# Kernel optimization log

Hardware: AMD Instinct MI355X
Metric: run time of the kernel (lower is better)

Reference implementation:

```python
import jax, jax.numpy as jnp
import numpy as np

TAU_M = 20.0
DT = 1.0
V_TH = 1.0
V_RESET = 0.0
ALPHA = float(np.exp(-DT / TAU_M))  # membrane decay per step

B, T, I, H, O = 64, 1024, 128, 512, 10


def spike_fn(v):
    # Heaviside spike; surrogate grad handled in fwdbwd module.
    return (v >= 0.0).astype(v.dtype)


def setup_inputs() -> dict:
    key = jax.random.key(0)
    k = jax.random.split(key, 6)
    x = jax.random.normal(k[0], (B, T, I), dtype=jnp.float32)
    # input_projection: Linear(I, H) -> weight [H, I], bias [H]
    Wi = jax.random.normal(k[1], (H, I), dtype=jnp.float32) * (1.0 / np.sqrt(I))
    bi = jnp.zeros((H,), dtype=jnp.float32)
    # recurrent weight [H, H] (xavier-ish)
    Wr = jax.random.normal(k[2], (H, H), dtype=jnp.float32) * float(np.sqrt(2.0 / (H + H)))
    # readout: Linear(H, O)
    Wo = jax.random.normal(k[3], (O, H), dtype=jnp.float32) * (1.0 / np.sqrt(H))
    bo = jnp.zeros((O,), dtype=jnp.float32)
    return {"x": x, "Wi": Wi, "bi": bi, "Wr": Wr, "Wo": Wo, "bo": bo}


def reference(x, Wi, bi, Wr, Wo, bo):
    # Precompute input projection for all timesteps: [B, T, H]
    x_proj = jnp.einsum('bti,hi->bth', x, Wi) + bi

    def step(carry, cur_t):
        h, spikes_prev = carry
        total_current = cur_t + spikes_prev @ Wr        # [B, H]
        h = ALPHA * h + total_current                    # LIF leak + integrate
        spikes = spike_fn(h - V_TH)                      # threshold
        h = spikes * V_RESET + (1.0 - spikes) * h        # reset on spike
        return (h, spikes), spikes

    h0 = jnp.zeros((x.shape[0], Wr.shape[0]), dtype=x.dtype)
    s0 = jnp.zeros_like(h0)
    (_, _), hidden_states = jax.lax.scan(step, (h0, s0), jnp.swapaxes(x_proj, 0, 1))
    hidden_states = jnp.swapaxes(hidden_states, 0, 1)    # [B, T, H]

    hidden_mean = hidden_states.mean(axis=1)             # rate readout
    output = hidden_mean @ Wo.T + bo                     # [B, O]
    return output, hidden_states
```

## Files before the change

### kernel.cpp

```cpp
#include <hip/hip_runtime.h>


#define ALPHA_F 0.951229424500714f

typedef unsigned int u32x4 __attribute__((ext_vector_type(4)));

__device__ float g_mean[64 * 512];

__global__ __launch_bounds__(256) void xproj_kernel(
    const float* __restrict__ x, const float* __restrict__ Wi,
    const float* __restrict__ bi, float* __restrict__ out)
{
    __shared__ float xs[64][132];
    __shared__ float ws[32][132];

    const int tid = threadIdx.x;
    const int bm = blockIdx.x;
    const int bn = blockIdx.y;

    const float* xb = x  + (size_t)bm * 64 * 128;
    const float* wb = Wi + (size_t)bn * 32 * 128;

    for (int l = 0; l < 8; ++l) {
        int idx = l * 256 + tid;
        int row = idx >> 5, c4 = idx & 31;
        *(float4*)(&xs[row][c4 * 4]) = *(const float4*)(xb + row * 128 + c4 * 4);
    }
    for (int l = 0; l < 4; ++l) {
        int idx = l * 256 + tid;
        int row = idx >> 5, c4 = idx & 31;
        *(float4*)(&ws[row][c4 * 4]) = *(const float4*)(wb + row * 128 + c4 * 4);
    }
    __syncthreads();

    const int txh = tid & 15, txm = tid >> 4;
    const int m0 = txm * 4, h0 = txh * 2;

    float4 acc[4][2];
    #pragma unroll
    for (int mm = 0; mm < 4; ++mm)
        #pragma unroll
        for (int q = 0; q < 2; ++q)
            acc[mm][q] = make_float4(0.f, 0.f, 0.f, 0.f);

    for (int k4 = 0; k4 < 32; ++k4) {
        float4 a[4], b[2];
        #pragma unroll
        for (int mm = 0; mm < 4; ++mm) a[mm] = *(const float4*)(&xs[m0 + mm][k4 * 4]);
        #pragma unroll
        for (int q = 0; q < 2; ++q)    b[q]  = *(const float4*)(&ws[h0 + q][k4 * 4]);
        #pragma unroll
        for (int mm = 0; mm < 4; ++mm) {
            #pragma unroll
            for (int q = 0; q < 2; ++q) {
                float p0 = a[mm].x * b[q].x;
                float p1 = a[mm].y * b[q].y;
                float p2 = a[mm].z * b[q].z;
                float p3 = a[mm].w * b[q].w;
                asm volatile("" : "+v"(p0), "+v"(p1), "+v"(p2), "+v"(p3));
                acc[mm][q].x += p0;
                acc[mm][q].y += p1;
                acc[mm][q].z += p2;
                acc[mm][q].w += p3;
            }
        }
    }

    const int hbase = bn * 32 + h0;
    #pragma unroll
    for (int mm = 0; mm < 4; ++mm) {
        size_t m = (size_t)bm * 64 + m0 + mm;
        float2 o;
        {
            float s01 = acc[mm][0].x + acc[mm][0].y;
            float s23 = acc[mm][0].z + acc[mm][0].w;
            float hs  = s01 + s23;
            o.x = hs + bi[hbase + 0];
        }
        {
            float s01 = acc[mm][1].x + acc[mm][1].y;
            float s23 = acc[mm][1].z + acc[mm][1].w;
            float hs  = s01 + s23;
            o.y = hs + bi[hbase + 1];
        }
        *(float2*)(&out[m * 512 + hbase]) = o;
    }
}

struct C8 { float a, b, c, d, e, f, g, h; };

__device__ __forceinline__ C8 fetch8v(const unsigned int* lst, int cidx,
                                      const char* wbase, int lane4) {
    u32x4 L0 = *(const u32x4*)(lst + cidx * 8);
    u32x4 L1 = *(const u32x4*)(lst + cidx * 8 + 4);
    C8 r;
    r.a = *(const float*)(wbase + (L0.x + lane4));
    r.b = *(const float*)(wbase + (L0.y + lane4));
    r.c = *(const float*)(wbase + (L0.z + lane4));
    r.d = *(const float*)(wbase + (L0.w + lane4));
    r.e = *(const float*)(wbase + (L1.x + lane4));
    r.f = *(const float*)(wbase + (L1.y + lane4));
    r.g = *(const float*)(wbase + (L1.z + lane4));
    r.h = *(const float*)(wbase + (L1.w + lane4));
    return r;
}

__device__ __forceinline__ void consume8(const C8& v, int e, int kA, int k,
                                         float& recA, float& recB) {
    if (e + 8 <= kA) {
        recA += v.a; recA += v.b; recA += v.c; recA += v.d;
        recA += v.e; recA += v.f; recA += v.g; recA += v.h;
    } else if (e >= kA && e + 8 <= k) {
        recB += v.a; recB += v.b; recB += v.c; recB += v.d;
        recB += v.e; recB += v.f; recB += v.g; recB += v.h;
    } else {
        if (e + 0 < k) { if (e + 0 < kA) recA += v.a; else recB += v.a; }
        if (e + 1 < k) { if (e + 1 < kA) recA += v.b; else recB += v.b; }
        if (e + 2 < k) { if (e + 2 < kA) recA += v.c; else recB += v.c; }
        if (e + 3 < k) { if (e + 3 < kA) recA += v.d; else recB += v.d; }
        if (e + 4 < k) { if (e + 4 < kA) recA += v.e; else recB += v.e; }
        if (e + 5 < k) { if (e + 5 < kA) recA += v.f; else recB += v.f; }
        if (e + 6 < k) { if (e + 6 < kA) recA += v.g; else recB += v.g; }
        if (e + 7 < k) { if (e + 7 < kA) recA += v.h; else recB += v.h; }
    }
}

__global__ __launch_bounds__(128, 1) void scan_kernel(
    const float* __restrict__ Wr, float* __restrict__ hid,
    u32x4* __restrict__ syn)
{
    const int blk  = blockIdx.x;
    const int p    = blk & 31;
    const int c    = blk >> 5;
    const int tid  = threadIdx.x;
    const int w    = tid >> 6;
    const int lane = tid & 63;
    const int s    = p + 32 * w;
    const int n    = (c << 6) + lane;
    const int lane4 = lane << 2;

    __shared__ float wrs[512][64];
    __shared__ alignas(16) unsigned int lists[2][512];
    __shared__ alignas(16) unsigned int maskbuf[2][16];

    #pragma unroll
    for (int i = 0; i < 8; ++i) ((unsigned int*)lists)[i * 128 + tid] = 0;

    {
        const float* src = Wr + (c << 6);
        for (int it = 0; it < 64; ++it) {
            int idx = it * 128 + tid;
            int r = idx >> 4, q = idx & 15;
            float4 v = *(const float4*)(src + (size_t)r * 512 + q * 4);
            *(float4*)(&wrs[r][q * 4]) = v;
        }
    }
    __syncthreads();

    unsigned int* list = lists[w];
    const char* wbase = (const char*)&wrs[0][0];
    float* base = hid + ((size_t)s * 1024) * 512 + n;

    float hstate = 0.0f;
    int cnt = 0;
    float xp = base[0];

    u32x4 prb0 = {0, 0, 0, 0}, prb1 = {0, 0, 0, 0};

    for (int t = 0; t < 1024; ++t) {
        int k = 0, kA = 0;
        if (t > 0) {
            const u32x4* pp = syn + ((((t - 1) & 1) * 64 + s) * 8) + (lane >> 3);
            asm volatile("s_waitcnt vmcnt(0)" ::: "memory");
            u32x4 pv;
            asm volatile("global_load_dwordx4 %0, %2, off sc0 sc1\n\t"
                         "global_load_dwordx4 %1, %2, off sc0 sc1"
                         : "+v"(prb0), "+v"(prb1) : "v"(pp) : "memory");
            for (;;) {
                asm volatile("s_waitcnt vmcnt(1)" : "+v"(prb0) :: "memory");
                unsigned long long ok = __ballot(prb0.z == (unsigned)t);
                if (ok == ~0ull) { pv = prb0; break; }
                asm volatile("global_load_dwordx4 %0, %1, off sc0 sc1"
                             : "+v"(prb0) : "v"(pp) : "memory");
                asm volatile("s_waitcnt vmcnt(1)" : "+v"(prb1) :: "memory");
                ok = __ballot(prb1.z == (unsigned)t);
                if (ok == ~0ull) { pv = prb1; break; }
                asm volatile("global_load_dwordx4 %0, %1, off sc0 sc1"
                             : "+v"(prb1) : "v"(pp) : "memory");
            }

            if ((lane & 7) == 0) {
                unsigned long long mword =
                    (((unsigned long long)pv.y) << 32) | (unsigned long long)pv.x;
                *(unsigned long long*)&maskbuf[w][(lane >> 3) * 2] = mword;
            }
            u32x4 r0 = *(const u32x4*)&maskbuf[w][0];
            u32x4 r1 = *(const u32x4*)&maskbuf[w][4];
            u32x4 r2 = *(const u32x4*)&maskbuf[w][8];
            u32x4 r3 = *(const u32x4*)&maskbuf[w][12];

            int p0 = __popc(r0.x), p1 = __popc(r0.y), p2 = __popc(r0.z), p3 = __popc(r0.w);
            int p4 = __popc(r1.x), p5 = __popc(r1.y), p6 = __popc(r1.z), p7 = __popc(r1.w);
            int p8 = __popc(r2.x), p9 = __popc(r2.y), p10 = __popc(r2.z), p11 = __popc(r2.w);
            int p12 = __popc(r3.x), p13 = __popc(r3.y), p14 = __popc(r3.z), p15 = __popc(r3.w);
            int ka_ = p0 + p1 + p2 + p3 + p4 + p5 + p6 + p7 + p8 + p9 + p10 + p11;
            int k_  = ka_ + p12 + p13 + p14 + p15;
            kA = __builtin_amdgcn_readfirstlane(ka_);
            k  = __builtin_amdgcn_readfirstlane(k_);

            const int myW = lane >> 2;
            int pre = 0;
            if (myW >  0) pre += p0;   if (myW >  1) pre += p1;
            if (myW >  2) pre += p2;   if (myW >  3) pre += p3;
            if (myW >  4) pre += p4;   if (myW >  5) pre += p5;
            if (myW >  6) pre += p6;   if (myW >  7) pre += p7;
            if (myW >  8) pre += p8;   if (myW >  9) pre += p9;
            if (myW > 10) pre += p10;  if (myW > 11) pre += p11;
            if (myW > 12) pre += p12;  if (myW > 13) pre += p13;
            if (myW > 14) pre += p14;
            unsigned word = (lane & 4) ? pv.y : pv.x;
            int shb = (lane & 3) * 8;
            pre += __popc(word & ((1u << shb) - 1u));
            unsigned byte = (word >> shb) & 0xFFu;

            int pos = pre;
            unsigned jbase = (unsigned)lane << 11;
            while (byte) {
                int bt = __builtin_ctz(byte);
                byte &= byte - 1u;
                list[pos++] = jbase + ((unsigned)bt << 8);
            }
        }

        float xp_next = base[(size_t)(t < 1023 ? t + 1 : 1023) * 512];

        float recA = 0.0f, recB = 0.0f;
        {
            int nch = (k + 7) >> 3;
            C8 b0, b1, b2;
            if (nch > 0) b0 = fetch8v(list, 0, wbase, lane4);
            if (nch > 1) b1 = fetch8v(list, 1, wbase, lane4);
            if (nch > 2) b2 = fetch8v(list, 2, wbase, lane4);
            int cc = 0;
            for (; cc + 6 <= nch; cc += 3) {
                consume8(b0, (cc + 0) * 8, kA, k, recA, recB); b0 = fetch8v(list, cc + 3, wbase, lane4);
                consume8(b1, (cc + 1) * 8, kA, k, recA, recB); b1 = fetch8v(list, cc + 4, wbase, lane4);
                consume8(b2, (cc + 2) * 8, kA, k, recA, recB); b2 = fetch8v(list, cc + 5, wbase, lane4);
            }
            int rem = nch - cc;
            if (rem >= 1) consume8(b0, (cc + 0) * 8, kA, k, recA, recB);
            if (rem >= 4) b0 = fetch8v(list, cc + 3, wbase, lane4);
            if (rem >= 2) consume8(b1, (cc + 1) * 8, kA, k, recA, recB);
            if (rem >= 5) b1 = fetch8v(list, cc + 4, wbase, lane4);
            if (rem >= 3) consume8(b2, (cc + 2) * 8, kA, k, recA, recB);
            if (rem >= 4) consume8(b0, (cc + 3) * 8, kA, k, recA, recB);
            if (rem >= 5) consume8(b1, (cc + 4) * 8, kA, k, recA, recB);
        }

        float rec = recA + recB;
        float cur = xp + rec;
        float tmp = ALPHA_F * hstate;
        asm volatile("" : "+v"(tmp));
        float hn = tmp + cur;
        bool sp = (hn >= 1.0f);
        hstate = sp ? 0.0f : hn;

        unsigned long long bm = __ballot(sp);
        if (lane == 0) {
            u32x4 pk;
            pk.x = (unsigned)bm; pk.y = (unsigned)(bm >> 32);
            pk.z = (unsigned)(t + 1); pk.w = 0u;
            u32x4* qp = syn + (((t & 1) * 64 + s) * 8) + c;
            asm volatile("global_store_dwordx4 %0, %1, off sc0 sc1"
                         :: "v"(qp), "v"(pk) : "memory");
        }

        base[(size_t)t * 512] = sp ? 1.0f : 0.0f;
        cnt += sp ? 1 : 0;
        xp = xp_next;
    }

    asm volatile("s_waitcnt vmcnt(0)" ::: "memory");
    asm volatile("" :: "v"(prb0), "v"(prb1));

    g_mean[s * 512 + n] = (float)cnt * (1.0f / 1024.0f);
}

__global__ __launch_bounds__(64) void readout_kernel(
    const float* __restrict__ Wo, const float* __restrict__ bo,
    float* __restrict__ out)
{
    const int b = blockIdx.x, o = blockIdx.y;
    const int lane = threadIdx.x;
    const float* mr = g_mean + b * 512;
    const float* wr = Wo + o * 512;
    double s = 0.0;
    for (int i = lane; i < 512; i += 64) s += (double)mr[i] * (double)wr[i];
    #pragma unroll
    for (int off = 32; off; off >>= 1) s += __shfl_down(s, off);
    if (lane == 0) out[b * 10 + o] = (float)(s + (double)bo[o]);
}

extern "C" void kernel_launch(void* const* d_in, const int* in_sizes, int n_in,
                              void* d_out, int out_size, void* d_ws, size_t ws_size,
                              hipStream_t stream) {
    const float* x  = (const float*)d_in[0];
    const float* Wi = (const float*)d_in[1];
    const float* bi = (const float*)d_in[2];
    const float* Wr = (const float*)d_in[3];
    const float* Wo = (const float*)d_in[4];
    const float* bo = (const float*)d_in[5];

    float* out = (float*)d_out;
    float* hid = out + 640;

    (void)hipMemsetAsync(d_ws, 0, 2 * 64 * 8 * 16, stream);

    dim3 gA(1024, 16);
    xproj_kernel<<<gA, 256, 0, stream>>>(x, Wi, bi, hid);

    scan_kernel<<<256, 128, 0, stream>>>(Wr, hid, (u32x4*)d_ws);

    dim3 gC(64, 10);
    readout_kernel<<<gC, 64, 0, stream>>>(Wo, bo, out);
}
```

Baseline: 2.100 ms.

## Speculatively prefetch spike flags and poll a cheaper-coherence mirror with sticky fallback

The cross-block spike-mask exchange is now written to two mirrors: one with sc0-only (narrower-scope) coherence and one with system-scope sc0 sc1. Readers issue the flag loads for the next step right after computing their own spikes, so the poll latency overlaps with the store and the next x-projection load. They first poll the cheaper mirror and switch permanently to the stronger-scope mirror after 64 failed tries. The x-projection load is also turned into an explicit asm prefetch waited on late. This adds a second store per step and relies on the narrower coherence scope eventually becoming visible across CUs, which may not hold on this hardware.

```diff
diff --git a/kernel.cpp b/kernel.cpp
--- a/kernel.cpp
+++ b/kernel.cpp
@@ -125,9 +125,14 @@
     }
 }
 
+#define ISSUE_FAST(P, A) \
+    asm volatile("global_load_dwordx4 %0, %1, off sc0" : "+v"(P) : "v"(A) : "memory")
+#define ISSUE_SLOW(P, A) \
+    asm volatile("global_load_dwordx4 %0, %1, off sc0 sc1" : "+v"(P) : "v"(A) : "memory")
+
 __global__ __launch_bounds__(128, 1) void scan_kernel(
     const float* __restrict__ Wr, float* __restrict__ hid,
-    u32x4* __restrict__ syn)
+    u32x4* __restrict__ synF)
 {
     const int blk  = blockIdx.x;
     const int p    = blk & 31;
@@ -139,6 +144,8 @@
     const int n    = (c << 6) + lane;
     const int lane4 = lane << 2;
 
+    u32x4* synS = synF + 2 * 64 * 8;
+
     __shared__ float wrs[512][64];
     __shared__ alignas(16) unsigned int lists[2][512];
     __shared__ alignas(16) unsigned int maskbuf[2][16];
@@ -163,30 +170,52 @@
 
     float hstate = 0.0f;
     int cnt = 0;
-    float xp = base[0];
+    bool sticky = false;
 
     u32x4 prb0 = {0, 0, 0, 0}, prb1 = {0, 0, 0, 0};
+    float xpn = 0.0f;
+
+    {
+        const float* xa = base;
+        asm volatile("global_load_dword %0, %1, off" : "+v"(xpn) : "v"(xa) : "memory");
+        asm volatile("s_waitcnt vmcnt(0)" : "+v"(xpn) :: "memory");
+    }
 
     for (int t = 0; t < 1024; ++t) {
         int k = 0, kA = 0;
         if (t > 0) {
-            const u32x4* pp = syn + ((((t - 1) & 1) * 64 + s) * 8) + (lane >> 3);
-            asm volatile("s_waitcnt vmcnt(0)" ::: "memory");
+            const int z0 = (t - 1) & 1;
             u32x4 pv;
-            asm volatile("global_load_dwordx4 %0, %2, off sc0 sc1\n\t"
-                         "global_load_dwordx4 %1, %2, off sc0 sc1"
-                         : "+v"(prb0), "+v"(prb1) : "v"(pp) : "memory");
-            for (;;) {
-                asm volatile("s_waitcnt vmcnt(1)" : "+v"(prb0) :: "memory");
-                unsigned long long ok = __ballot(prb0.z == (unsigned)t);
-                if (ok == ~0ull) { pv = prb0; break; }
-                asm volatile("global_load_dwordx4 %0, %1, off sc0 sc1"
-                             : "+v"(prb0) : "v"(pp) : "memory");
-                asm volatile("s_waitcnt vmcnt(1)" : "+v"(prb1) :: "memory");
-                ok = __ballot(prb1.z == (unsigned)t);
-                if (ok == ~0ull) { pv = prb1; break; }
-                asm volatile("global_load_dwordx4 %0, %1, off sc0 sc1"
-                             : "+v"(prb1) : "v"(pp) : "memory");
+            bool got = false;
+            asm volatile("s_waitcnt vmcnt(5)" : "+v"(prb0) :: "memory");
+            if (__ballot(prb0.z == (unsigned)t) == ~0ull) { pv = prb0; got = true; }
+            if (!got) {
+                asm volatile("s_waitcnt vmcnt(4)" : "+v"(prb1) :: "memory");
+                if (__ballot(prb1.z == (unsigned)t) == ~0ull) { pv = prb1; got = true; }
+            }
+            if (!got) {
+                asm volatile("s_waitcnt vmcnt(0)" ::: "memory");
+                const u32x4* ppF = synF + ((z0 * 64 + s) * 8) + (lane >> 3);
+                const u32x4* ppS = synS + ((z0 * 64 + s) * 8) + (lane >> 3);
+                int tries = 0;
+                for (;;) {
+                    if (!sticky) { ISSUE_FAST(prb0, ppF); ISSUE_FAST(prb1, ppF); }
+                    else         { ISSUE_SLOW(prb0, ppS); ISSUE_SLOW(prb1, ppS); }
+                    bool done = false, swtch = false;
+                    for (;;) {
+                        asm volatile("s_waitcnt vmcnt(1)" : "+v"(prb0) :: "memory");
+                        if (__ballot(prb0.z == (unsigned)t) == ~0ull) { pv = prb0; done = true; break; }
+                        if (!sticky && ++tries >= 64) { swtch = true; break; }
+                        if (!sticky) ISSUE_FAST(prb0, ppF); else ISSUE_SLOW(prb0, ppS);
+                        asm volatile("s_waitcnt vmcnt(1)" : "+v"(prb1) :: "memory");
+                        if (__ballot(prb1.z == (unsigned)t) == ~0ull) { pv = prb1; done = true; break; }
+                        if (!sticky && ++tries >= 64) { swtch = true; break; }
+                        if (!sticky) ISSUE_FAST(prb1, ppF); else ISSUE_SLOW(prb1, ppS);
+                    }
+                    if (done) break;
+                    if (swtch) { sticky = true; asm volatile("s_waitcnt vmcnt(0)" ::: "memory"); }
+                }
+                asm volatile("s_waitcnt vmcnt(0)" ::: "memory");
             }
 
             if ((lane & 7) == 0) {
@@ -232,8 +261,6 @@
             }
         }
 
-        float xp_next = base[(size_t)(t < 1023 ? t + 1 : 1023) * 512];
-
         float recA = 0.0f, recB = 0.0f;
         {
             int nch = (k + 7) >> 3;
@@ -257,31 +284,58 @@
             if (rem >= 5) consume8(b1, (cc + 4) * 8, kA, k, recA, recB);
         }
 
+        asm volatile("s_waitcnt vmcnt(0)" : "+v"(xpn) :: "memory");
+        float xpv = xpn;
+
         float rec = recA + recB;
-        float cur = xp + rec;
+        float cur = xpv + rec;
         float tmp = ALPHA_F * hstate;
         asm volatile("" : "+v"(tmp));
         float hn = tmp + cur;
         bool sp = (hn >= 1.0f);
         hstate = sp ? 0.0f : hn;
+        cnt += sp ? 1 : 0;
 
         unsigned long long bm = __ballot(sp);
+
+        const int z = t & 1;
+        {
+            if (!sticky) {
+                const u32x4* pp = synF + ((z * 64 + s) * 8) + (lane >> 3);
+                asm volatile("global_load_dwordx4 %0, %2, off sc0\n\t"
+                             "global_load_dwordx4 %1, %2, off sc0"
+                             : "+v"(prb0), "+v"(prb1) : "v"(pp) : "memory");
+            } else {
+                const u32x4* pp = synS + ((z * 64 + s) * 8) + (lane >> 3);
+                asm volatile("global_load_dwordx4 %0, %2, off sc0 sc1\n\t"
+                             "global_load_dwordx4 %1, %2, off sc0 sc1"
+                             : "+v"(prb0), "+v"(prb1) : "v"(pp) : "memory");
+            }
+        }
         if (lane == 0) {
             u32x4 pk;
             pk.x = (unsigned)bm; pk.y = (unsigned)(bm >> 32);
             pk.z = (unsigned)(t + 1); pk.w = 0u;
-            u32x4* qp = syn + (((t & 1) * 64 + s) * 8) + c;
+            u32x4* qF = synF + ((z * 64 + s) * 8) + c;
+            u32x4* qS = synS + ((z * 64 + s) * 8) + c;
+            asm volatile("global_store_dwordx4 %0, %1, off sc0"
+                         :: "v"(qF), "v"(pk) : "memory");
             asm volatile("global_store_dwordx4 %0, %1, off sc0 sc1"
-                         :: "v"(qp), "v"(pk) : "memory");
-        }
-
-        base[(size_t)t * 512] = sp ? 1.0f : 0.0f;
-        cnt += sp ? 1 : 0;
-        xp = xp_next;
+                         :: "v"(qS), "v"(pk) : "memory");
+        }
+        {
+            float spv = sp ? 1.0f : 0.0f;
+            float* spa = base + (size_t)t * 512;
+            asm volatile("global_store_dword %0, %1, off" :: "v"(spa), "v"(spv) : "memory");
+        }
+        {
+            const float* xa = base + (size_t)(t < 1023 ? t + 1 : 1023) * 512;
+            asm volatile("global_load_dword %0, %1, off" : "+v"(xpn) : "v"(xa) : "memory");
+        }
     }
 
     asm volatile("s_waitcnt vmcnt(0)" ::: "memory");
-    asm volatile("" :: "v"(prb0), "v"(prb1));
+    asm volatile("" :: "v"(prb0), "v"(prb1), "v"(xpn));
 
     g_mean[s * 512 + n] = (float)cnt * (1.0f / 1024.0f);
 }
@@ -314,7 +368,7 @@
     float* out = (float*)d_out;
     float* hid = out + 640;
 
-    (void)hipMemsetAsync(d_ws, 0, 2 * 64 * 8 * 16, stream);
+    (void)hipMemsetAsync(d_ws, 0, 2 * (2 * 64 * 8 * 16), stream);
 
     dim3 gA(1024, 16);
     xproj_kernel<<<gA, 256, 0, stream>>>(x, Wi, bi, hid);
```

Measured after the change: 2.856 ms. +36.0%, slower.

## Replace polled dwordx4 flag loads with 64-bit atomics and speculative prefetch

Applied to the files above, without the earlier changes.

The inter-block spike exchange now uses 64-bit atomic swaps to publish each half-mask tagged with the timestep, and atomic-OR-with-zero reads to poll it. The first poll is issued speculatively right after publishing, so it overlaps with the next step's input load. A sleep-backed retry loop runs only when the speculative read is stale. This aims to cut the latency of the per-timestep cross-block handshake, at the cost of atomic traffic and tighter correctness requirements on ordering.

```diff
diff --git a/kernel.cpp b/kernel.cpp
--- a/kernel.cpp
+++ b/kernel.cpp
@@ -127,7 +127,7 @@
 
 __global__ __launch_bounds__(128, 1) void scan_kernel(
     const float* __restrict__ Wr, float* __restrict__ hid,
-    u32x4* __restrict__ syn)
+    unsigned long long* __restrict__ syn)
 {
     const int blk  = blockIdx.x;
     const int p    = blk & 31;
@@ -163,35 +163,47 @@
 
     float hstate = 0.0f;
     int cnt = 0;
-    float xp = base[0];
-
-    u32x4 prb0 = {0, 0, 0, 0}, prb1 = {0, 0, 0, 0};
+
+    unsigned long long pa0 = 0ull, pb0 = 0ull;
+    float xpn = 0.0f;
+    unsigned long long zq = 0ull;
+
+    {
+        const float* xa = base;
+        asm volatile("global_load_dword %0, %1, off" : "+v"(xpn) : "v"(xa) : "memory");
+        asm volatile("s_waitcnt vmcnt(0)" : "+v"(xpn) :: "memory");
+    }
 
     for (int t = 0; t < 1024; ++t) {
         int k = 0, kA = 0;
         if (t > 0) {
-            const u32x4* pp = syn + ((((t - 1) & 1) * 64 + s) * 8) + (lane >> 3);
-            asm volatile("s_waitcnt vmcnt(0)" ::: "memory");
-            u32x4 pv;
-            asm volatile("global_load_dwordx4 %0, %2, off sc0 sc1\n\t"
-                         "global_load_dwordx4 %1, %2, off sc0 sc1"
-                         : "+v"(prb0), "+v"(prb1) : "v"(pp) : "memory");
-            for (;;) {
-                asm volatile("s_waitcnt vmcnt(1)" : "+v"(prb0) :: "memory");
-                unsigned long long ok = __ballot(prb0.z == (unsigned)t);
-                if (ok == ~0ull) { pv = prb0; break; }
-                asm volatile("global_load_dwordx4 %0, %1, off sc0 sc1"
-                             : "+v"(prb0) : "v"(pp) : "memory");
-                asm volatile("s_waitcnt vmcnt(1)" : "+v"(prb1) :: "memory");
-                ok = __ballot(prb1.z == (unsigned)t);
-                if (ok == ~0ull) { pv = prb1; break; }
-                asm volatile("global_load_dwordx4 %0, %1, off sc0 sc1"
-                             : "+v"(prb1) : "v"(pp) : "memory");
+            asm volatile("s_waitcnt vmcnt(0)" : "+v"(pa0), "+v"(pb0), "+v"(xpn) :: "memory");
+            bool c0 = ((lane & 7) != 0) ||
+                      ((unsigned)(pa0 >> 32) == (unsigned)t &&
+                       (unsigned)(pb0 >> 32) == (unsigned)t);
+            if (__ballot(c0) != ~0ull) {
+                const int z0 = (t - 1) & 1;
+                unsigned long long* ra = syn + ((z0 * 64 + s) * 8 + (lane >> 3)) * 2;
+                for (;;) {
+                    if ((lane & 7) == 0) {
+                        asm volatile("global_atomic_or_x2 %0, %2, %4, off sc0\n\t"
+                                     "global_atomic_or_x2 %1, %3, %4, off sc0"
+                                     : "+v"(pa0), "+v"(pb0)
+                                     : "v"(ra), "v"(ra + 1), "v"(zq) : "memory");
+                    }
+                    asm volatile("s_waitcnt vmcnt(0)" : "+v"(pa0), "+v"(pb0) :: "memory");
+                    bool cc = ((lane & 7) != 0) ||
+                              ((unsigned)(pa0 >> 32) == (unsigned)t &&
+                               (unsigned)(pb0 >> 32) == (unsigned)t);
+                    if (__ballot(cc) == ~0ull) break;
+                    __builtin_amdgcn_s_sleep(1);
+                }
             }
 
             if ((lane & 7) == 0) {
                 unsigned long long mword =
-                    (((unsigned long long)pv.y) << 32) | (unsigned long long)pv.x;
+                    (unsigned long long)(unsigned)pa0 |
+                    ((unsigned long long)(unsigned)pb0 << 32);
                 *(unsigned long long*)&maskbuf[w][(lane >> 3) * 2] = mword;
             }
             u32x4 r0 = *(const u32x4*)&maskbuf[w][0];
@@ -218,7 +230,7 @@
             if (myW > 10) pre += p10;  if (myW > 11) pre += p11;
             if (myW > 12) pre += p12;  if (myW > 13) pre += p13;
             if (myW > 14) pre += p14;
-            unsigned word = (lane & 4) ? pv.y : pv.x;
+            unsigned word = ((const unsigned*)&maskbuf[w][0])[myW];
             int shb = (lane & 3) * 8;
             pre += __popc(word & ((1u << shb) - 1u));
             unsigned byte = (word >> shb) & 0xFFu;
@@ -231,8 +243,6 @@
                 list[pos++] = jbase + ((unsigned)bt << 8);
             }
         }
-
-        float xp_next = base[(size_t)(t < 1023 ? t + 1 : 1023) * 512];
 
         float recA = 0.0f, recB = 0.0f;
         {
@@ -257,31 +267,49 @@
             if (rem >= 5) consume8(b1, (cc + 4) * 8, kA, k, recA, recB);
         }
 
+        float xpv = xpn;
+
         float rec = recA + recB;
-        float cur = xp + rec;
+        float cur = xpv + rec;
         float tmp = ALPHA_F * hstate;
         asm volatile("" : "+v"(tmp));
         float hn = tmp + cur;
         bool sp = (hn >= 1.0f);
         hstate = sp ? 0.0f : hn;
+        cnt += sp ? 1 : 0;
 
         unsigned long long bm = __ballot(sp);
+
+        const int z = t & 1;
         if (lane == 0) {
-            u32x4 pk;
-            pk.x = (unsigned)bm; pk.y = (unsigned)(bm >> 32);
-            pk.z = (unsigned)(t + 1); pk.w = 0u;
-            u32x4* qp = syn + (((t & 1) * 64 + s) * 8) + c;
-            asm volatile("global_store_dwordx4 %0, %1, off sc0 sc1"
-                         :: "v"(qp), "v"(pk) : "memory");
-        }
-
-        base[(size_t)t * 512] = sp ? 1.0f : 0.0f;
-        cnt += sp ? 1 : 0;
-        xp = xp_next;
+            unsigned long long w0 =
+                ((unsigned long long)(unsigned)(t + 1) << 32) | (unsigned)bm;
+            unsigned long long w1 =
+                ((unsigned long long)(unsigned)(t + 1) << 32) | (unsigned)(bm >> 32);
+            unsigned long long* ro = syn + ((z * 64 + s) * 8 + c) * 2;
+            asm volatile("global_atomic_swap_x2 %0, %1, off" :: "v"(ro), "v"(w0) : "memory");
+            asm volatile("global_atomic_swap_x2 %0, %1, off" :: "v"(ro + 1), "v"(w1) : "memory");
+        }
+        {
+            float spv = sp ? 1.0f : 0.0f;
+            float* spa = base + (size_t)t * 512;
+            asm volatile("global_store_dword %0, %1, off" :: "v"(spa), "v"(spv) : "memory");
+        }
+        {
+            const float* xa = base + (size_t)(t < 1023 ? t + 1 : 1023) * 512;
+            asm volatile("global_load_dword %0, %1, off" : "+v"(xpn) : "v"(xa) : "memory");
+        }
+        if ((lane & 7) == 0) {
+            unsigned long long* ra = syn + ((z * 64 + s) * 8 + (lane >> 3)) * 2;
+            asm volatile("global_atomic_or_x2 %0, %2, %4, off sc0\n\t"
+                         "global_atomic_or_x2 %1, %3, %4, off sc0"
+                         : "+v"(pa0), "+v"(pb0)
+                         : "v"(ra), "v"(ra + 1), "v"(zq) : "memory");
+        }
     }
 
     asm volatile("s_waitcnt vmcnt(0)" ::: "memory");
-    asm volatile("" :: "v"(prb0), "v"(prb1));
+    asm volatile("" :: "v"(pa0), "v"(pb0), "v"(xpn), "v"(zq));
 
     g_mean[s * 512 + n] = (float)cnt * (1.0f / 1024.0f);
 }
@@ -319,7 +347,7 @@
     dim3 gA(1024, 16);
     xproj_kernel<<<gA, 256, 0, stream>>>(x, Wi, bi, hid);
 
-    scan_kernel<<<256, 128, 0, stream>>>(Wr, hid, (u32x4*)d_ws);
+    scan_kernel<<<256, 128, 0, stream>>>(Wr, hid, (unsigned long long*)d_ws);
 
     dim3 gC(64, 10);
     readout_kernel<<<gC, 64, 0, stream>>>(Wo, bo, out);
```

Result: slower. 2.259 ms (+7.6%).

## Issue next-step spike-flag polls and x-projection load right after publishing spikes

Applied to the files above, without the earlier changes.

At the end of each timestep, right after storing its spike mask, the recurrence kernel now issues the next step's x-projection load and two speculative polls of the peer spike-mask slots, using explicit asm loads. This lets the cross-workgroup handshake latency overlap with the remaining tail work. The slow polling loop only runs if neither early probe already holds the expected step tag. The spike-word extraction now reads from shared memory rather than from the probe register. The cost is tighter manual vmcnt ordering, which leaves the loads fragile to reordering.

```diff
diff --git a/kernel.cpp b/kernel.cpp
--- a/kernel.cpp
+++ b/kernel.cpp
@@ -163,30 +163,43 @@
 
     float hstate = 0.0f;
     int cnt = 0;
-    float xp = base[0];
 
     u32x4 prb0 = {0, 0, 0, 0}, prb1 = {0, 0, 0, 0};
+    float xpn = 0.0f;
+
+    {
+        const float* xa = base;
+        asm volatile("global_load_dword %0, %1, off" : "+v"(xpn) : "v"(xa) : "memory");
+        asm volatile("s_waitcnt vmcnt(0)" : "+v"(xpn) :: "memory");
+    }
 
     for (int t = 0; t < 1024; ++t) {
         int k = 0, kA = 0;
         if (t > 0) {
-            const u32x4* pp = syn + ((((t - 1) & 1) * 64 + s) * 8) + (lane >> 3);
-            asm volatile("s_waitcnt vmcnt(0)" ::: "memory");
             u32x4 pv;
-            asm volatile("global_load_dwordx4 %0, %2, off sc0 sc1\n\t"
-                         "global_load_dwordx4 %1, %2, off sc0 sc1"
-                         : "+v"(prb0), "+v"(prb1) : "v"(pp) : "memory");
-            for (;;) {
-                asm volatile("s_waitcnt vmcnt(1)" : "+v"(prb0) :: "memory");
-                unsigned long long ok = __ballot(prb0.z == (unsigned)t);
-                if (ok == ~0ull) { pv = prb0; break; }
-                asm volatile("global_load_dwordx4 %0, %1, off sc0 sc1"
-                             : "+v"(prb0) : "v"(pp) : "memory");
-                asm volatile("s_waitcnt vmcnt(1)" : "+v"(prb1) :: "memory");
-                ok = __ballot(prb1.z == (unsigned)t);
-                if (ok == ~0ull) { pv = prb1; break; }
-                asm volatile("global_load_dwordx4 %0, %1, off sc0 sc1"
-                             : "+v"(prb1) : "v"(pp) : "memory");
+            bool got = false;
+            asm volatile("s_waitcnt vmcnt(1)" : "+v"(prb0), "+v"(xpn) :: "memory");
+            if (__ballot(prb0.z == (unsigned)t) == ~0ull) { pv = prb0; got = true; }
+            if (!got) {
+                asm volatile("s_waitcnt vmcnt(0)" : "+v"(prb1) :: "memory");
+                if (__ballot(prb1.z == (unsigned)t) == ~0ull) { pv = prb1; got = true; }
+            }
+            if (!got) {
+                const int z0 = (t - 1) & 1;
+                const u32x4* pp = syn + ((z0 * 64 + s) * 8) + (lane >> 3);
+                asm volatile("global_load_dwordx4 %0, %2, off sc0 sc1\n\t"
+                             "global_load_dwordx4 %1, %2, off sc0 sc1"
+                             : "+v"(prb0), "+v"(prb1) : "v"(pp) : "memory");
+                for (;;) {
+                    asm volatile("s_waitcnt vmcnt(1)" : "+v"(prb0) :: "memory");
+                    if (__ballot(prb0.z == (unsigned)t) == ~0ull) { pv = prb0; break; }
+                    asm volatile("global_load_dwordx4 %0, %1, off sc0 sc1"
+                                 : "+v"(prb0) : "v"(pp) : "memory");
+                    asm volatile("s_waitcnt vmcnt(1)" : "+v"(prb1) :: "memory");
+                    if (__ballot(prb1.z == (unsigned)t) == ~0ull) { pv = prb1; break; }
+                    asm volatile("global_load_dwordx4 %0, %1, off sc0 sc1"
+                                 : "+v"(prb1) : "v"(pp) : "memory");
+                }
             }
 
             if ((lane & 7) == 0) {
@@ -218,7 +231,7 @@
             if (myW > 10) pre += p10;  if (myW > 11) pre += p11;
             if (myW > 12) pre += p12;  if (myW > 13) pre += p13;
             if (myW > 14) pre += p14;
-            unsigned word = (lane & 4) ? pv.y : pv.x;
+            unsigned word = ((const unsigned*)&maskbuf[w][0])[myW];
             int shb = (lane & 3) * 8;
             pre += __popc(word & ((1u << shb) - 1u));
             unsigned byte = (word >> shb) & 0xFFu;
@@ -231,8 +244,6 @@
                 list[pos++] = jbase + ((unsigned)bt << 8);
             }
         }
-
-        float xp_next = base[(size_t)(t < 1023 ? t + 1 : 1023) * 512];
 
         float recA = 0.0f, recB = 0.0f;
         {
@@ -257,31 +268,47 @@
             if (rem >= 5) consume8(b1, (cc + 4) * 8, kA, k, recA, recB);
         }
 
+        float xpv = xpn;
+
         float rec = recA + recB;
-        float cur = xp + rec;
+        float cur = xpv + rec;
         float tmp = ALPHA_F * hstate;
         asm volatile("" : "+v"(tmp));
         float hn = tmp + cur;
         bool sp = (hn >= 1.0f);
         hstate = sp ? 0.0f : hn;
+        cnt += sp ? 1 : 0;
 
         unsigned long long bm = __ballot(sp);
+
+        const int z = t & 1;
         if (lane == 0) {
             u32x4 pk;
             pk.x = (unsigned)bm; pk.y = (unsigned)(bm >> 32);
             pk.z = (unsigned)(t + 1); pk.w = 0u;
-            u32x4* qp = syn + (((t & 1) * 64 + s) * 8) + c;
+            u32x4* qp = syn + ((z * 64 + s) * 8) + c;
             asm volatile("global_store_dwordx4 %0, %1, off sc0 sc1"
                          :: "v"(qp), "v"(pk) : "memory");
         }
-
-        base[(size_t)t * 512] = sp ? 1.0f : 0.0f;
-        cnt += sp ? 1 : 0;
-        xp = xp_next;
+        {
+            float spv = sp ? 1.0f : 0.0f;
+            float* spa = base + (size_t)t * 512;
+            asm volatile("global_store_dword %0, %1, off" :: "v"(spa), "v"(spv) : "memory");
+        }
+        {
+            const float* xa = base + (size_t)(t < 1023 ? t + 1 : 1023) * 512;
+            asm volatile("global_load_dword %0, %1, off" : "+v"(xpn) : "v"(xa) : "memory");
+        }
+        {
+            const u32x4* pp = syn + ((z * 64 + s) * 8) + (lane >> 3);
+            asm volatile("global_load_dwordx4 %0, %2, off sc0 sc1\n\t"
+                         "global_load_dwordx4 %1, %2, off sc0 sc1"
+                         : "+v"(prb0), "+v"(prb1) : "v"(pp) : "memory");
+        }
     }
 
     asm volatile("s_waitcnt vmcnt(0)" ::: "memory");
-    asm volatile("" :: "v"(prb0), "v"(prb1));
+    asm volatile("" :: "v"(prb0), "v"(prb1), "v"(xpn));
 
     g_mean[s * 512 + n] = (float)cnt * (1.0f / 1024.0f);
 }
```

After: 2.238 ms. 6.6% more time.
